# Kernel optimization log

Hardware: AMD Instinct MI355X
Metric: run time of the kernel (lower is better)

## Reference

```python
import jax, jax.numpy as jnp
import numpy as np
from jax import lax

T = 1.0
B = 262144
STEPS = 20


def proj2manifold(x):
    # Polar-type retraction via SVD: nearest orthogonal matrix.
    u, _, vT = jnp.linalg.svd(x, full_matrices=False)
    return u @ vT


def setup_inputs() -> dict:
    key = jax.random.key(0)
    k1, k2, k3 = jax.random.split(key, 3)
    # Initial state: random matrices projected onto SO(3)/O(3).
    x0 = proj2manifold(jax.random.normal(k1, (B, 3, 3), dtype=jnp.float32))
    # Per-sample integration horizon t in (0, T].
    t = jax.random.uniform(k2, (B, 1), dtype=jnp.float32, minval=1e-3, maxval=T)
    # Pre-drawn Brownian increments (unit Gaussians), one per step.
    noise = jax.random.normal(k3, (STEPS, B, 3, 3), dtype=jnp.float32)
    return {"x": x0, "t": t, "noise": noise, "steps": STEPS}


def reference(x, t, noise, steps):
    # t: [B,1] -> [B,1,1]  (mirrors t.unsqueeze(2) in sample())
    dt = (t / steps)[:, :, None]           # [B,1,1]
    sqrt_dt = jnp.sqrt(dt)                 # [B,1,1]

    def step(xc, eps):
        inc = sqrt_dt * eps                # tangent-space Gaussian increment
        # proj2tangent: 0.5 * (v - x v^T x); drift f(x,t) = 0
        v = 0.5 * (inc - xc @ jnp.swapaxes(inc, -1, -2) @ xc)
        xn = proj2manifold(xc + v)         # SVD retraction back to manifold
        return xn, None

    xf, _ = lax.scan(step, x, noise)
    return xf
```

## Files before the change

### kernel.cpp

```cpp
#include <hip/hip_runtime.h>

#define TPB 256
typedef float v4fa __attribute__((ext_vector_type(4), aligned(4)));

#define NTS(v, p)  __builtin_nontemporal_store((v), (p))

__device__ __forceinline__ void so3_step(float x[9], const float e[9], float hs) {
    float wa = 0.f, wb = 0.f, wc = 0.f;
    #pragma unroll
    for (int k = 0; k < 3; ++k) {
        const float xk0 = x[k*3+0], xk1 = x[k*3+1], xk2 = x[k*3+2];
        const float ek0 = e[k*3+0], ek1 = e[k*3+1], ek2 = e[k*3+2];
        wa += xk2*ek1 - xk1*ek2;
        wb += xk0*ek2 - xk2*ek0;
        wc += xk1*ek0 - xk0*ek1;
    }
    const float A  = hs * wa;
    const float Bv = hs * wb;
    const float Cv = hs * wc;

    const float th2 = A*A + Bv*Bv + Cv*Cv;
    const float c1  = rsqrtf(1.0f + th2);
    const float c2  = c1*c1 / (1.0f + c1);

    const float q00 = 1.0f - c2*(Bv*Bv + Cv*Cv);
    const float q11 = 1.0f - c2*(A*A  + Cv*Cv);
    const float q22 = 1.0f - c2*(A*A  + Bv*Bv);
    const float q01 = c2*A*Bv  - c1*Cv;
    const float q10 = c2*A*Bv  + c1*Cv;
    const float q02 = c2*A*Cv  + c1*Bv;
    const float q20 = c2*A*Cv  - c1*Bv;
    const float q12 = c2*Bv*Cv - c1*A;
    const float q21 = c2*Bv*Cv + c1*A;

    #pragma unroll
    for (int r = 0; r < 3; ++r) {
        const float a0 = x[r*3+0], a1 = x[r*3+1], a2 = x[r*3+2];
        x[r*3+0] = a0*q00 + a1*q10 + a2*q20;
        x[r*3+1] = a0*q01 + a1*q11 + a2*q21;
        x[r*3+2] = a0*q02 + a1*q12 + a2*q22;
    }
}

__device__ __forceinline__ void load9(const float* __restrict__ p, float e[9]) {
    v4fa lo = *(const v4fa*)(p);
    v4fa hi = *(const v4fa*)(p + 4);
    e[0] = lo.x; e[1] = lo.y; e[2] = lo.z; e[3] = lo.w;
    e[4] = hi.x; e[5] = hi.y; e[6] = hi.z; e[7] = hi.w;
    e[8] = p[8];
}

__global__ __launch_bounds__(TPB) void brownian_so3_kernel(
    const float* __restrict__ x0,
    const float* __restrict__ t,
    const float* __restrict__ noise,
    float* __restrict__ out,
    int B, int steps)
{
    const int b = blockIdx.x * TPB + threadIdx.x;

    const float tv = t[b];

    float x[9];
    load9(x0 + (long)b * 9, x);

    const long stride = (long)B * 9;
    const float* np = noise + (long)b * 9;

    float cur[9], nxt[9];
    load9(np, cur);
    if (steps > 1) load9(np + stride, nxt);

    const float hs = 0.5f * sqrtf(tv / (float)steps);

    for (int s = 0; s < steps; ++s) {
        float e[9];
        #pragma unroll
        for (int j = 0; j < 9; ++j) e[j] = cur[j];
        #pragma unroll
        for (int j = 0; j < 9; ++j) cur[j] = nxt[j];
        if (s + 2 < steps) load9(np + (long)(s + 2) * stride, cur);
        so3_step(x, e, hs);
        #pragma unroll
        for (int j = 0; j < 9; ++j) { float tmp = cur[j]; cur[j] = nxt[j]; nxt[j] = tmp; }
    }

    float* op = out + (long)b * 9;
    v4fa lo, hi;
    lo.x = x[0]; lo.y = x[1]; lo.z = x[2]; lo.w = x[3];
    hi.x = x[4]; hi.y = x[5]; hi.z = x[6]; hi.w = x[7];
    NTS(lo, (v4fa*)op);
    NTS(hi, (v4fa*)(op + 4));
    NTS(x[8], op + 8);
}

extern "C" void kernel_launch(void* const* d_in, const int* in_sizes, int n_in,
                              void* d_out, int out_size, void* d_ws, size_t ws_size,
                              hipStream_t stream) {
    const float* x0    = (const float*)d_in[0];
    const float* t     = (const float*)d_in[1];
    const float* noise = (const float*)d_in[2];
    float* out = (float*)d_out;

    const int B     = in_sizes[0] / 9;
    const int steps = in_sizes[2] / in_sizes[0];

    const int grid = B / TPB;
    brownian_so3_kernel<<<grid, TPB, 0, stream>>>(x0, t, noise, out, B, steps);
}
```

Before: 37.69 us.

## Stage noise and state through per-wave LDS for coalesced 16-byte global loads

Replaces the per-thread strided 9-float loads, which are misaligned for vector access, with wave-cooperative coalesced float4 loads of each wave's contiguous 64×9 block. The data is staged into double-buffered LDS and each lane then reads its 9 values back out. Output is transposed through LDS the same way before coalesced nontemporal stores. Global access efficiency should improve, at the cost of LDS traffic, possible bank conflicts from the stride-9 reads, extra registers for prefetch, and wave-barrier ordering.

```diff
diff --git a/kernel.cpp b/kernel.cpp
--- a/kernel.cpp
+++ b/kernel.cpp
@@ -1,9 +1,11 @@
 #include <hip/hip_runtime.h>
 
 #define TPB 256
-typedef float v4fa __attribute__((ext_vector_type(4), aligned(4)));
+#define WPB 4
+typedef float v4f __attribute__((ext_vector_type(4)));
 
 #define NTS(v, p)  __builtin_nontemporal_store((v), (p))
+#define WBAR()     __builtin_amdgcn_wave_barrier()
 
 __device__ __forceinline__ void so3_step(float x[9], const float e[9], float hs) {
     float wa = 0.f, wb = 0.f, wc = 0.f;
@@ -42,14 +44,6 @@
     }
 }
 
-__device__ __forceinline__ void load9(const float* __restrict__ p, float e[9]) {
-    v4fa lo = *(const v4fa*)(p);
-    v4fa hi = *(const v4fa*)(p + 4);
-    e[0] = lo.x; e[1] = lo.y; e[2] = lo.z; e[3] = lo.w;
-    e[4] = hi.x; e[5] = hi.y; e[6] = hi.z; e[7] = hi.w;
-    e[8] = p[8];
-}
-
 __global__ __launch_bounds__(TPB) void brownian_so3_kernel(
     const float* __restrict__ x0,
     const float* __restrict__ t,
@@ -57,41 +51,107 @@
     float* __restrict__ out,
     int B, int steps)
 {
-    const int b = blockIdx.x * TPB + threadIdx.x;
+    __shared__ v4f lds[2][WPB][144];
+
+    const int tid  = threadIdx.x;
+    const int wave = tid >> 6;
+    const int lane = tid & 63;
+    const int sbase = (blockIdx.x * WPB + wave) * 64;
+    const int b     = sbase + lane;
+    const long fbase  = (long)sbase * 9;
+    const long stride = (long)B * 9;
 
     const float tv = t[b];
 
+    v4f* buf0 = &lds[0][wave][0];
+    v4f* buf1 = &lds[1][wave][0];
+    const float* f0 = (const float*)buf0;
+    const float* f1 = (const float*)buf1;
+
+    {
+        const v4f* src = (const v4f*)(x0 + fbase);
+        buf0[lane]      = src[lane];
+        buf0[lane + 64] = src[lane + 64];
+        if (lane < 16) buf0[lane + 128] = src[lane + 128];
+    }
+    WBAR();
     float x[9];
-    load9(x0 + (long)b * 9, x);
-
-    const long stride = (long)B * 9;
-    const float* np = noise + (long)b * 9;
-
-    float cur[9], nxt[9];
-    load9(np, cur);
-    if (steps > 1) load9(np + stride, nxt);
+    #pragma unroll
+    for (int j = 0; j < 9; ++j) x[j] = f0[lane*9 + j];
+    WBAR();
 
     const float hs = 0.5f * sqrtf(tv / (float)steps);
 
-    for (int s = 0; s < steps; ++s) {
-        float e[9];
-        #pragma unroll
-        for (int j = 0; j < 9; ++j) e[j] = cur[j];
-        #pragma unroll
-        for (int j = 0; j < 9; ++j) cur[j] = nxt[j];
-        if (s + 2 < steps) load9(np + (long)(s + 2) * stride, cur);
-        so3_step(x, e, hs);
-        #pragma unroll
-        for (int j = 0; j < 9; ++j) { float tmp = cur[j]; cur[j] = nxt[j]; nxt[j] = tmp; }
+    v4f A0, A1, A2, B0, B1, B2;
+    A2 = (v4f)0.f; B2 = (v4f)0.f; B0 = (v4f)0.f; B1 = (v4f)0.f;
+    {
+        const v4f* src = (const v4f*)(noise + fbase);
+        A0 = src[lane]; A1 = src[lane + 64];
+        if (lane < 16) A2 = src[lane + 128];
+    }
+    if (steps > 1) {
+        const v4f* src = (const v4f*)(noise + stride + fbase);
+        B0 = src[lane]; B1 = src[lane + 64];
+        if (lane < 16) B2 = src[lane + 128];
+    }
+    buf0[lane] = A0; buf0[lane + 64] = A1;
+    if (lane < 16) buf0[lane + 128] = A2;
+    if (steps > 2) {
+        const v4f* src = (const v4f*)(noise + 2*stride + fbase);
+        A0 = src[lane]; A1 = src[lane + 64];
+        if (lane < 16) A2 = src[lane + 128];
     }
 
-    float* op = out + (long)b * 9;
-    v4fa lo, hi;
-    lo.x = x[0]; lo.y = x[1]; lo.z = x[2]; lo.w = x[3];
-    hi.x = x[4]; hi.y = x[5]; hi.z = x[6]; hi.w = x[7];
-    NTS(lo, (v4fa*)op);
-    NTS(hi, (v4fa*)(op + 4));
-    NTS(x[8], op + 8);
+    float e[9];
+    int s = 0;
+    for (; s + 1 < steps; s += 2) {
+        {
+            buf1[lane] = B0; buf1[lane + 64] = B1;
+            if (lane < 16) buf1[lane + 128] = B2;
+        }
+        if (s + 3 < steps) {
+            const v4f* src = (const v4f*)(noise + (long)(s+3)*stride + fbase);
+            B0 = src[lane]; B1 = src[lane + 64];
+            if (lane < 16) B2 = src[lane + 128];
+        }
+        #pragma unroll
+        for (int j = 0; j < 9; ++j) e[j] = f0[lane*9 + j];
+        so3_step(x, e, hs);
+        WBAR();
+
+        if (s + 2 < steps) {
+            buf0[lane] = A0; buf0[lane + 64] = A1;
+            if (lane < 16) buf0[lane + 128] = A2;
+        }
+        if (s + 4 < steps) {
+            const v4f* src = (const v4f*)(noise + (long)(s+4)*stride + fbase);
+            A0 = src[lane]; A1 = src[lane + 64];
+            if (lane < 16) A2 = src[lane + 128];
+        }
+        #pragma unroll
+        for (int j = 0; j < 9; ++j) e[j] = f1[lane*9 + j];
+        so3_step(x, e, hs);
+        WBAR();
+    }
+    if (s < steps) {
+        #pragma unroll
+        for (int j = 0; j < 9; ++j) e[j] = f0[lane*9 + j];
+        so3_step(x, e, hs);
+    }
+
+    WBAR();
+    {
+        float* ob = (float*)buf0;
+        #pragma unroll
+        for (int j = 0; j < 9; ++j) ob[lane*9 + j] = x[j];
+    }
+    WBAR();
+    {
+        v4f* dst = (v4f*)(out + fbase);
+        NTS(buf0[lane],      dst + lane);
+        NTS(buf0[lane + 64], dst + lane + 64);
+        if (lane < 16) NTS(buf0[lane + 128], dst + lane + 128);
+    }
 }
 
 extern "C" void kernel_launch(void* const* d_in, const int* in_sizes, int n_in,
```

New measurement: 39.06 us. +3.6%, slower.
